# Performance work log

Measured on AMD Instinct MI355X. Metric: run time of the kernel, lower is better.

## Reference

```python
import jax, jax.numpy as jnp
import numpy as np

B, N, E = 4, 10000, 160000
F_EXOG = 8
IN_DIM = 9          # 1 (pm25) + F_EXOG
HIST, PRED = 8, 12
HID = 64
GNN_OUT = 13
E_HID, E_OUT = 32, 30
GRU_IN = IN_DIM + GNN_OUT  # 22


def setup_inputs() -> dict:
    key = jax.random.key(0)
    ks = jax.random.split(key, 16)
    s = 0.1
    return {
        "pm25_hist": jax.random.normal(ks[0], (B, HIST, N, 1), jnp.float32),
        "feature": jax.random.normal(ks[1], (B, HIST + PRED, N, F_EXOG), jnp.float32),
        "edge_attr": jax.random.uniform(ks[2], (E, 2), jnp.float32),
        "wind_mean": jnp.array([2.0, 180.0], jnp.float32),
        "wind_std": jnp.array([1.5, 90.0], jnp.float32),
        # edge MLP: Linear(21->32), Sigmoid, Linear(32->30), Sigmoid
        "e_w1": jax.random.normal(ks[3], (2 * IN_DIM + 3, E_HID), jnp.float32) * s,
        "e_b1": jnp.zeros((E_HID,), jnp.float32),
        "e_w2": jax.random.normal(ks[4], (E_HID, E_OUT), jnp.float32) * s,
        "e_b2": jnp.zeros((E_OUT,), jnp.float32),
        # node MLP: Linear(30->13), Sigmoid
        "n_w": jax.random.normal(ks[5], (E_OUT, GNN_OUT), jnp.float32) * s,
        "n_b": jnp.zeros((GNN_OUT,), jnp.float32),
        # GRUCell(22 -> 64), torch layout: weight_ih (3H, in), weight_hh (3H, H)
        "gru_wi": jax.random.normal(ks[6], (3 * HID, GRU_IN), jnp.float32) * s,
        "gru_wh": jax.random.normal(ks[7], (3 * HID, HID), jnp.float32) * s,
        "gru_bi": jnp.zeros((3 * HID,), jnp.float32),
        "gru_bh": jnp.zeros((3 * HID,), jnp.float32),
        # fc_out: Linear(64 -> 1)
        "fc_w": jax.random.normal(ks[8], (HID, 1), jnp.float32) * s,
        "fc_b": jnp.zeros((1,), jnp.float32),
        "edge_index": jax.random.randint(ks[9], (2, E), 0, N, jnp.int64),
    }


def _forward(pm25_hist, feature, edge_attr, wind_mean, wind_std,
             e_w1, e_b1, e_w2, e_b2, n_w, n_b,
             gru_wi, gru_wh, gru_bi, gru_bh, fc_w, fc_b, edge_index):
    batch, _, n_nodes, _ = pm25_hist.shape
    src, tgt = edge_index[0], edge_index[1]

    # buffers precomputed in __init__ (torch.std uses ddof=1)
    edge_mean = edge_attr.mean(axis=0, keepdims=True)
    edge_std = jnp.maximum(jnp.std(edge_attr, axis=0, ddof=1, keepdims=True), 1e-6)
    edge_attr_norm = (edge_attr - edge_mean) / edge_std          # (E, 2)
    city_dist = jnp.maximum(edge_attr[:, 0], 1e-3)               # (E,)
    city_direc = edge_attr[:, 1]                                 # (E,)
    w_std = jnp.maximum(wind_std, 1e-6)

    def graph_gnn(x):                                            # x: (B, N, IN_DIM)
        node_src = x[:, src]                                     # (B, E, IN_DIM)
        node_tgt = x[:, tgt]
        wind = node_src[..., -2:] * w_std + wind_mean            # de-normalize
        speed = jnp.maximum(wind[..., 0], 0.0)                   # (B, E)
        wdir = jnp.deg2rad(wind[..., 1])
        theta = jnp.abs(city_direc - wdir)
        edge_w = jax.nn.relu(3.0 * speed * jnp.cos(theta) / city_dist)  # (B, E)
        ean = jnp.broadcast_to(edge_attr_norm, (x.shape[0], E, 2))
        h = jnp.concatenate([node_src, node_tgt, ean, edge_w[..., None]], axis=-1)
        h = jax.nn.sigmoid(h @ e_w1 + e_b1)
        h = jax.nn.sigmoid(h @ e_w2 + e_b2)                      # (B, E, E_OUT)
        agg = jnp.zeros((x.shape[0], n_nodes, E_OUT), x.dtype)
        agg = agg.at[:, tgt].add(h).at[:, src].add(-h)           # scatter add / sub
        return jax.nn.sigmoid(agg @ n_w + n_b)                   # (B, N, GNN_OUT)

    def gru_step(h, x):                                          # h,x: (B*N, .)
        gi = x @ gru_wi.T + gru_bi
        gh = h @ gru_wh.T + gru_bh
        i_r, i_z, i_n = jnp.split(gi, 3, axis=-1)
        h_r, h_z, h_n = jnp.split(gh, 3, axis=-1)
        r = jax.nn.sigmoid(i_r + h_r)
        z = jax.nn.sigmoid(i_z + h_z)
        n = jnp.tanh(i_n + r * h_n)
        return (1.0 - z) * n + z * h

    def step(carry, feat_t):
        hn, xn = carry                                           # (B*N,HID), (B,N,1)
        x = jnp.concatenate([xn, feat_t], axis=-1)               # (B, N, IN_DIM)
        x_gnn = graph_gnn(x)
        xc = jnp.concatenate([x_gnn, x], axis=-1).reshape(batch * n_nodes, -1)
        hn = gru_step(hn, xc)
        xn = hn.reshape(batch, n_nodes, HID) @ fc_w + fc_b       # (B, N, 1)
        return (hn, xn), xn[..., 0]

    hn0 = jnp.zeros((batch * n_nodes, HID), pm25_hist.dtype)
    xn0 = pm25_hist[:, -1]                                       # (B, N, 1)
    feats = jnp.swapaxes(feature[:, HIST:HIST + PRED], 0, 1)     # (PRED, B, N, F)
    _, preds = jax.lax.scan(step, (hn0, xn0), feats)             # (PRED, B, N)
    return jnp.transpose(preds, (1, 2, 0))                       # (B, N, PRED)


def reference(pm25_hist, feature, edge_attr, wind_mean, wind_std,
              e_w1, e_b1, e_w2, e_b2, n_w, n_b,
              gru_wi, gru_wh, gru_bi, gru_bh, fc_w, fc_b, edge_index):
    return _forward(pm25_hist, feature, edge_attr, wind_mean, wind_std,
                    e_w1, e_b1, e_w2, e_b2, n_w, n_b,
                    gru_wi, gru_wh, gru_bi, gru_bh, fc_w, fc_b, edge_index)
```

## Files before the change

kernel.cpp:

```cpp
#include <hip/hip_runtime.h>
#include <hip/hip_fp16.h>
#include <cstddef>

#define BB    4
#define NN    10000
#define EE    160000
#define BN    40000
#define HISTC 8
#define PREDC 12
#define TSTEP 20
#define FEX   8
#define HIDC  64
#define EHID  32
#define EOUTC 30
#define GOUTC 13
#define GINC  22

typedef float v2f __attribute__((ext_vector_type(2)));
typedef _Float16 v2h __attribute__((ext_vector_type(2)));

struct alignas(16) WPack {
    __half2 w[16];
    float   nw[14];
    float   b2;
    float   pad;
};

__device__ __forceinline__ float fast_rcp(float x) { return __builtin_amdgcn_rcpf(x); }
__device__ __forceinline__ float sigm(float x) {
    return fast_rcp(1.0f + __expf(-x));
}
__device__ __forceinline__ v2f sigm2(v2f x) {
    v2f r; r.x = sigm(x.x); r.y = sigm(x.y); return r;
}
__device__ __forceinline__ float tanh_fast(float x) {
    x = fminf(fmaxf(x, -15.0f), 15.0f);
    float e = __expf(2.0f * x);
    return (e - 1.0f) * fast_rcp(e + 1.0f);
}

__device__ __forceinline__ float dot2(__half2 a, __half2 b, float c) {
#if __has_builtin(__builtin_amdgcn_fdot2)
    union { __half2 h; v2h v; } ua, ub;
    ua.h = a; ub.h = b;
    return __builtin_amdgcn_fdot2(ua.v, ub.v, c, false);
#else
    float2 fa = __half22float2(a), fb = __half22float2(b);
    return c + fa.x * fb.x + fa.y * fb.y;
#endif
}

__global__ __launch_bounds__(256) void stats1_kernel(const float* __restrict__ ea,
                                                     double* __restrict__ part) {
    __shared__ double sm[256][4];
    int tid = threadIdx.x;
    double s0 = 0, s1 = 0, q0 = 0, q1 = 0;
    for (int e = blockIdx.x * 256 + tid; e < EE; e += 256 * 256) {
        float2 v = reinterpret_cast<const float2*>(ea)[e];
        double v0 = (double)v.x, v1 = (double)v.y;
        s0 += v0; q0 += v0 * v0;
        s1 += v1; q1 += v1 * v1;
    }
    sm[tid][0] = s0; sm[tid][1] = s1; sm[tid][2] = q0; sm[tid][3] = q1;
    __syncthreads();
    for (int off = 128; off > 0; off >>= 1) {
        if (tid < off)
            for (int k = 0; k < 4; k++) sm[tid][k] += sm[tid + off][k];
        __syncthreads();
    }
    if (tid == 0) {
        part[blockIdx.x * 4 + 0] = sm[0][0];
        part[blockIdx.x * 4 + 1] = sm[0][1];
        part[blockIdx.x * 4 + 2] = sm[0][2];
        part[blockIdx.x * 4 + 3] = sm[0][3];
    }
}

__global__ __launch_bounds__(256) void stats2_kernel(const double* __restrict__ part,
                                                     float* __restrict__ stats) {
    __shared__ double sm[256][4];
    int tid = threadIdx.x;
    sm[tid][0] = part[tid * 4 + 0];
    sm[tid][1] = part[tid * 4 + 1];
    sm[tid][2] = part[tid * 4 + 2];
    sm[tid][3] = part[tid * 4 + 3];
    __syncthreads();
    for (int off = 128; off > 0; off >>= 1) {
        if (tid < off)
            for (int k = 0; k < 4; k++) sm[tid][k] += sm[tid + off][k];
        __syncthreads();
    }
    if (tid == 0) {
        double m0 = sm[0][0] / EE, m1 = sm[0][1] / EE;
        double v0 = (sm[0][2] - sm[0][0] * sm[0][0] / EE) / (double)(EE - 1);
        double v1 = (sm[0][3] - sm[0][1] * sm[0][1] / EE) / (double)(EE - 1);
        float sd0 = fmaxf((float)sqrt(v0 > 0 ? v0 : 0.0), 1e-6f);
        float sd1 = fmaxf((float)sqrt(v1 > 0 ? v1 : 0.0), 1e-6f);
        stats[0] = (float)m0; stats[1] = (float)m1;
        stats[2] = 1.0f / sd0; stats[3] = 1.0f / sd1;
    }
}

__global__ __launch_bounds__(256) void edgepre_kernel(
    const float* __restrict__ ea, const float* __restrict__ stats,
    const int* __restrict__ eidx,
    int* __restrict__ deg_t, int* __restrict__ deg_s,
    float4* __restrict__ epre4)
{
    int e = blockIdx.x * 256 + threadIdx.x;
    if (e >= EE) return;
    float2 v = reinterpret_cast<const float2*>(ea)[e];
    float4 r;
    r.x = (v.x - stats[0]) * stats[2];
    r.y = (v.y - stats[1]) * stats[3];
    r.z = 1.0f / fmaxf(v.x, 1e-3f);
    r.w = v.y;
    epre4[e] = r;
    atomicAdd(&deg_s[eidx[e]], 1);
    atomicAdd(&deg_t[eidx[EE + e]], 1);
}

__global__ __launch_bounds__(256) void cvtw_kernel(
    const float* __restrict__ wi, const float* __restrict__ wh,
    const float* __restrict__ ew2, const float* __restrict__ eb2,
    const float* __restrict__ nw,
    __half* __restrict__ wi_h, __half* __restrict__ wh_h,
    WPack* __restrict__ wpack)
{
    int i = blockIdx.x * 256 + threadIdx.x;
    if (i < 192 * GINC) wi_h[i] = __float2half(wi[i]);
    if (i < 192 * HIDC) wh_h[i] = __float2half(wh[i]);
    if (i < EOUTC) {
        WPack wp;
        #pragma unroll
        for (int q = 0; q < 16; q++)
            wp.w[q] = __floats2half2_rn(ew2[(2 * q) * EOUTC + i],
                                        ew2[(2 * q + 1) * EOUTC + i]);
        #pragma unroll
        for (int j = 0; j < GOUTC; j++) wp.nw[j] = nw[i * GOUTC + j];
        wp.nw[13] = 0.f;
        wp.b2 = eb2[i];
        wp.pad = 0.f;
        wpack[i] = wp;
    }
}

__global__ void initxn_kernel(const float* __restrict__ pm, float* __restrict__ xn) {
    int i = blockIdx.x * 256 + threadIdx.x;
    if (i >= BN) return;
    int b = i / NN, n = i - b * NN;
    xn[i] = pm[(b * HISTC + (HISTC - 1)) * NN + n];
}

__global__ __launch_bounds__(1024) void scan_kernel(
    const int* __restrict__ deg_t, const int* __restrict__ deg_s,
    int* __restrict__ off_t, int* __restrict__ off_s,
    int* __restrict__ cnt_t, int* __restrict__ cnt_s)
{
    __shared__ int pt[1024], ps[1024];
    int tid = threadIdx.x;
    int base = tid * 10;
    int st = 0, ss = 0;
    for (int k = 0; k < 10; k++) {
        int i = base + k;
        if (i < NN) { st += deg_t[i]; ss += deg_s[i]; }
    }
    pt[tid] = st; ps[tid] = ss;
    __syncthreads();
    for (int off = 1; off < 1024; off <<= 1) {
        int vt = (tid >= off) ? pt[tid - off] : 0;
        int vs = (tid >= off) ? ps[tid - off] : 0;
        __syncthreads();
        pt[tid] += vt; ps[tid] += vs;
        __syncthreads();
    }
    int ext = (tid == 0) ? 0 : pt[tid - 1];
    int exs = (tid == 0) ? 0 : ps[tid - 1];
    for (int k = 0; k < 10; k++) {
        int i = base + k;
        if (i < NN) {
            off_t[i] = ext; cnt_t[i] = ext;
            off_s[i] = exs; cnt_s[i] = exs;
            ext += deg_t[i]; exs += deg_s[i];
        }
    }
    if (tid == 0) { off_t[NN] = EE; off_s[NN] = EE; }
}

__global__ void fillperm_kernel(const int* __restrict__ eidx,
                                const float4* __restrict__ epre4,
                                int* __restrict__ cnt_t, int* __restrict__ cnt_s,
                                int4* __restrict__ eT, float4* __restrict__ epreT)
{
    int e = blockIdx.x * 256 + threadIdx.x;
    if (e >= EE) return;
    int s = eidx[e];
    int g = eidx[EE + e];
    int pt = atomicAdd(&cnt_t[g], 1);
    int ps = atomicAdd(&cnt_s[s], 1);
    int4 r; r.x = s; r.y = g; r.z = ps; r.w = 0;
    eT[pt] = r;
    epreT[pt] = epre4[e];
}

__global__ __launch_bounds__(256) void featpre_kernel(
    const float* __restrict__ feature,
    const float* __restrict__ ew1,
    const float* __restrict__ wmean, const float* __restrict__ wstd,
    __half* __restrict__ preSfeat, __half* __restrict__ preTfeat,
    float2* __restrict__ wind2all)
{
    __shared__ alignas(16) float w1s[18 * EHID];
    for (int i = threadIdx.x; i < 18 * EHID; i += 256) w1s[i] = ew1[i];
    __syncthreads();
    int idx = blockIdx.x * 256 + threadIdx.x;
    if (idx >= BN * 8 * PREDC) return;
    int c  = idx & 7;
    int r2 = idx >> 3;
    int t  = r2 / BN;
    int i  = r2 - t * BN;
    int b = i / NN, n = i - b * NN;
    float xf[8];
    {
        const float4* fp = reinterpret_cast<const float4*>(
            feature + (((size_t)b * TSTEP + HISTC + t) * NN + n) * FEX);
        float4 u = fp[0], v = fp[1];
        xf[0] = u.x; xf[1] = u.y; xf[2] = u.z; xf[3] = u.w;
        xf[4] = v.x; xf[5] = v.y; xf[6] = v.z; xf[7] = v.w;
    }
    float4 aS = {0.f, 0.f, 0.f, 0.f}, aT = {0.f, 0.f, 0.f, 0.f};
    #pragma unroll
    for (int k = 0; k < 8; k++) {
        float4 wS = reinterpret_cast<const float4*>(&w1s[(k + 1) * EHID])[c];
        float4 wT = reinterpret_cast<const float4*>(&w1s[(10 + k) * EHID])[c];
        aS.x += xf[k] * wS.x; aS.y += xf[k] * wS.y; aS.z += xf[k] * wS.z; aS.w += xf[k] * wS.w;
        aT.x += xf[k] * wT.x; aT.y += xf[k] * wT.y; aT.z += xf[k] * wT.z; aT.w += xf[k] * wT.w;
    }
    union { uint2 u; __half h[4]; } sv, tv;
    sv.h[0] = __float2half(aS.x); sv.h[1] = __float2half(aS.y);
    sv.h[2] = __float2half(aS.z); sv.h[3] = __float2half(aS.w);
    tv.h[0] = __float2half(aT.x); tv.h[1] = __float2half(aT.y);
    tv.h[2] = __float2half(aT.z); tv.h[3] = __float2half(aT.w);
    size_t base = ((size_t)t * BN + i) * EHID;
    reinterpret_cast<uint2*>(preSfeat + base)[c] = sv.u;
    reinterpret_cast<uint2*>(preTfeat + base)[c] = tv.u;
    if (c == 1) {
        float sd0 = fmaxf(wstd[0], 1e-6f), sd1 = fmaxf(wstd[1], 1e-6f);
        float speed = fmaxf(xf[6] * sd0 + wmean[0], 0.f);
        float wdir  = (xf[7] * sd1 + wmean[1]) * 0.017453292519943295f;
        float2 wv; wv.x = 3.0f * speed; wv.y = wdir;
        wind2all[(size_t)t * BN + i] = wv;
    }
}

__global__ __launch_bounds__(256) void edge_kernel(
    const int4* __restrict__ eT, const float4* __restrict__ epreT,
    const __half* __restrict__ preSfeat, const __half* __restrict__ preTfeat,
    const float2* __restrict__ wind2all, int t,
    const float* __restrict__ xncur,
    const float* __restrict__ ew1, const float* __restrict__ eb1,
    const WPack* __restrict__ wpack,
    __half* __restrict__ h3t, __half* __restrict__ h3s)
{
    int i = blockIdx.x * 256 + threadIdx.x;
    int b = blockIdx.y;
    int4 et = eT[i];
    int s = et.x, g = et.y, ps = et.z;
    float4 ep = epreT[i];

    size_t iS = (size_t)b * NN + s, iT = (size_t)b * NN + g;
    size_t tb = (size_t)t * BN;
    float2 wv2 = wind2all[tb + iS];
    float ew = fmaxf(wv2.x * __cosf(fabsf(ep.w - wv2.y)) * ep.z, 0.f);
    float xnS = xncur[iS], xnT = xncur[iT];

    union alignas(16) { uint4 u[4]; __half2 h2[16]; } RS, RT;
    {
        const uint4* p;
        p = reinterpret_cast<const uint4*>(preSfeat + (tb + iS) * EHID);
        RS.u[0] = p[0]; RS.u[1] = p[1]; RS.u[2] = p[2]; RS.u[3] = p[3];
        p = reinterpret_cast<const uint4*>(preTfeat + (tb + iT) * EHID);
        RT.u[0] = p[0]; RT.u[1] = p[1]; RT.u[2] = p[2]; RT.u[3] = p[3];
    }

    const v2f* W00 = reinterpret_cast<const v2f*>(ew1);
    const v2f* W09 = reinterpret_cast<const v2f*>(ew1 + 9 * EHID);
    const v2f* W18 = reinterpret_cast<const v2f*>(ew1 + 18 * EHID);
    const v2f* W19 = reinterpret_cast<const v2f*>(ew1 + 19 * EHID);
    const v2f* W20 = reinterpret_cast<const v2f*>(ew1 + 20 * EHID);
    const v2f* B1  = reinterpret_cast<const v2f*>(eb1);
    float ean0 = ep.x, ean1 = ep.y;
    __half2 h1h[16];
    #pragma unroll
    for (int q = 0; q < 16; q++) {
        v2f u = W18[q] * ean0 + W19[q] * ean1 + B1[q] + W20[q] * ew
              + W00[q] * xnS + W09[q] * xnT;
        float2 rs = __half22float2(RS.h2[q]);
        float2 rt = __half22float2(RT.h2[q]);
        u.x += rs.x + rt.x;
        u.y += rs.y + rt.y;
        v2f sg = sigm2(u);
        h1h[q] = __floats2half2_rn(sg.x, sg.y);
    }

    v2f h3p[7];
    #pragma unroll
    for (int j = 0; j < 7; j++) { h3p[j].x = 0.f; h3p[j].y = 0.f; }
    for (int o = 0; o < EOUTC; o++) {
        const WPack* W = wpack + o;
        float acc0 = W->b2, acc1 = 0.f;
        #pragma unroll
        for (int q = 0; q < 16; q += 2) {
            acc0 = dot2(h1h[q],     W->w[q],     acc0);
            acc1 = dot2(h1h[q + 1], W->w[q + 1], acc1);
        }
        float h2v = sigm(acc0 + acc1);
        const v2f* nr = reinterpret_cast<const v2f*>(W->nw);
        #pragma unroll
        for (int j = 0; j < 7; j++) h3p[j] += nr[j] * h2v;
    }

    union alignas(16) { uint4 u[2]; __half2 h2[8]; } r;
    #pragma unroll
    for (int j = 0; j < 7; j++) r.h2[j] = __floats2half2_rn(h3p[j].x, h3p[j].y);
    r.h2[7] = __floats2half2_rn(0.f, 0.f);
    {
        __half* oT = h3t + ((size_t)b * EE + i) * 16;
        reinterpret_cast<uint4*>(oT)[0] = r.u[0];
        reinterpret_cast<uint4*>(oT)[1] = r.u[1];
        __half* oS = h3s + ((size_t)b * EE + ps) * 16;
        reinterpret_cast<uint4*>(oS)[0] = r.u[0];
        reinterpret_cast<uint4*>(oS)[1] = r.u[1];
    }
}

__global__ __launch_bounds__(256) void gathernode_kernel(
    const __half* __restrict__ h3t, const __half* __restrict__ h3s,
    const int* __restrict__ off_t, const int* __restrict__ off_s,
    const float* __restrict__ nb,
    const float* __restrict__ feature, int t,
    const __half* __restrict__ wi_h, const __half* __restrict__ wh_h,
    const float* __restrict__ bi, const float* __restrict__ bh,
    const float* __restrict__ fw, const float* __restrict__ fb,
    const __half2* __restrict__ hnold, __half2* __restrict__ hnnew,
    float* __restrict__ xncur, float* __restrict__ out)
{
    __shared__ alignas(16) __half xcs[16][4][16];
    __shared__ float xpart[4][64];
    int tid = threadIdx.x;
    int n0 = blockIdx.x * 16;

    {
        int l = tid & 63;
        int gb = l >> 4, ch = l & 15;
        int wv = tid >> 6;
        const __half* ht = h3t + (size_t)gb * ((size_t)EE * 16) + ch;
        const __half* hs = h3s + (size_t)gb * ((size_t)EE * 16) + ch;
        for (int rr = 0; rr < 4; rr++) {
            int ln = rr * 4 + wv;
            int n = __builtin_amdgcn_readfirstlane(n0 + ln);
            float a0 = 0.f, a1 = 0.f, a2 = 0.f, a3 = 0.f;
            {
                int i0 = off_t[n], i1 = off_t[n + 1];
                int i = i0;
                for (; i + 4 <= i1; i += 4) {
                    a0 += __half2float(ht[(size_t)(i + 0) * 16]);
                    a1 += __half2float(ht[(size_t)(i + 1) * 16]);
                    a2 += __half2float(ht[(size_t)(i + 2) * 16]);
                    a3 += __half2float(ht[(size_t)(i + 3) * 16]);
                }
                for (; i < i1; i++) a0 += __half2float(ht[(size_t)i * 16]);
            }
            {
                int i0 = off_s[n], i1 = off_s[n + 1];
                int i = i0;
                for (; i + 4 <= i1; i += 4) {
                    a0 -= __half2float(hs[(size_t)(i + 0) * 16]);
                    a1 -= __half2float(hs[(size_t)(i + 1) * 16]);
                    a2 -= __half2float(hs[(size_t)(i + 2) * 16]);
                    a3 -= __half2float(hs[(size_t)(i + 3) * 16]);
                }
                for (; i < i1; i++) a0 -= __half2float(hs[(size_t)i * 16]);
            }
            float acc = (a0 + a1) + (a2 + a3);
            __half v = (ch < GOUTC) ? __float2half(sigm(acc + nb[ch]))
                                    : __float2half(0.f);
            xcs[ln][gb][ch] = v;
        }
    }
    __syncthreads();

    int lane = tid & 63, wav = tid >> 6;
    int nn = lane & 15, b = lane >> 4;
    int node = b * NN + n0 + nn;
    float xn_old = xncur[node];

    __half2 xch[11];
    {
        const __half2* xp2 = reinterpret_cast<const __half2*>(&xcs[nn][b][0]);
        #pragma unroll
        for (int p = 0; p < 6; p++) xch[p] = xp2[p];
        xch[6] = __halves2half2(xcs[nn][b][12], __float2half(xn_old));
    }
    {
        const float4* fp = reinterpret_cast<const float4*>(
            feature + (((size_t)b * TSTEP + HISTC + t) * NN + (n0 + nn)) * FEX);
        float4 u = fp[0], v = fp[1];
        xch[7]  = __floats2half2_rn(u.x, u.y);
        xch[8]  = __floats2half2_rn(u.z, u.w);
        xch[9]  = __floats2half2_rn(v.x, v.y);
        xch[10] = __floats2half2_rn(v.z, v.w);
    }

    __half2 hh[32];
    #pragma unroll
    for (int p = 0; p < 32; p++) hh[p] = hnold[(size_t)p * BN + node];

    float xsum = 0.f;
    for (int jb = 0; jb < 4; jb++) {
        #pragma unroll
        for (int jj2 = 0; jj2 < 2; jj2++) {
            int j0 = __builtin_amdgcn_readfirstlane(jb * 16 + wav * 4 + jj2 * 2);
            union { __half2 h; __half v[2]; } holdw;
            holdw.h = hnold[(size_t)(j0 >> 1) * BN + node];
            float hnew2[2];
            #pragma unroll
            for (int d = 0; d < 2; d++) {
                int j = j0 + d;
                float ir = bi[j], iz = bi[64 + j], in_ = bi[128 + j];
                const __half2* wr0 = reinterpret_cast<const __half2*>(wi_h + (size_t)j * GINC);
                const __half2* wr1 = reinterpret_cast<const __half2*>(wi_h + (size_t)(64 + j) * GINC);
                const __half2* wr2 = reinterpret_cast<const __half2*>(wi_h + (size_t)(128 + j) * GINC);
                #pragma unroll
                for (int p = 0; p < 11; p++) {
                    ir  = dot2(xch[p], wr0[p], ir);
                    iz  = dot2(xch[p], wr1[p], iz);
                    in_ = dot2(xch[p], wr2[p], in_);
                }
                float hr0 = bh[j], hz0 = bh[64 + j], hn0 = bh[128 + j];
                float hr1 = 0.f, hz1 = 0.f, hn1 = 0.f;
                const __half2* vr0 = reinterpret_cast<const __half2*>(wh_h + (size_t)j * HIDC);
                const __half2* vr1 = reinterpret_cast<const __half2*>(wh_h + (size_t)(64 + j) * HIDC);
                const __half2* vr2 = reinterpret_cast<const __half2*>(wh_h + (size_t)(128 + j) * HIDC);
                #pragma unroll
                for (int p = 0; p < 32; p += 2) {
                    hr0 = dot2(hh[p],     vr0[p],     hr0);
                    hz0 = dot2(hh[p],     vr1[p],     hz0);
                    hn0 = dot2(hh[p],     vr2[p],     hn0);
                    hr1 = dot2(hh[p + 1], vr0[p + 1], hr1);
                    hz1 = dot2(hh[p + 1], vr1[p + 1], hz1);
                    hn1 = dot2(hh[p + 1], vr2[p + 1], hn1);
                }
                float r  = sigm(ir + hr0 + hr1);
                float z  = sigm(iz + hz0 + hz1);
                float nl = tanh_fast(in_ + r * (hn0 + hn1));
                float hold = __half2float(holdw.v[d]);
                float hnew = (1.f - z) * nl + z * hold;
                hnew2[d] = hnew;
                xsum += hnew * fw[j];
            }
            hnnew[(size_t)(j0 >> 1) * BN + node] = __floats2half2_rn(hnew2[0], hnew2[1]);
        }
    }
    xpart[wav][lane] = xsum;
    __syncthreads();
    if (wav == 0) {
        float tot = xpart[0][lane] + xpart[1][lane] + xpart[2][lane] + xpart[3][lane];
        float xnew = tot + fb[0];
        xncur[node] = xnew;
        out[(size_t)node * PREDC + t] = xnew;
    }
}

extern "C" void kernel_launch(void* const* d_in, const int* in_sizes, int n_in,
                              void* d_out, int out_size, void* d_ws, size_t ws_size,
                              hipStream_t stream)
{
    const float* pm    = (const float*)d_in[0];
    const float* feat  = (const float*)d_in[1];
    const float* ea    = (const float*)d_in[2];
    const float* wmean = (const float*)d_in[3];
    const float* wstd  = (const float*)d_in[4];
    const float* ew1   = (const float*)d_in[5];
    const float* eb1   = (const float*)d_in[6];
    const float* ew2   = (const float*)d_in[7];
    const float* eb2   = (const float*)d_in[8];
    const float* nw    = (const float*)d_in[9];
    const float* nb    = (const float*)d_in[10];
    const float* wi    = (const float*)d_in[11];
    const float* wh    = (const float*)d_in[12];
    const float* bi    = (const float*)d_in[13];
    const float* bh    = (const float*)d_in[14];
    const float* fw    = (const float*)d_in[15];
    const float* fb    = (const float*)d_in[16];
    const int*   eidx  = (const int*)d_in[17];
    float* out = (float*)d_out;

    char* w = (char*)d_ws;
    double* partd = (double*)w;                    w += 256 * 4 * sizeof(double);
    float*  stats = (float*)w;                     w += 16 * sizeof(float);
    WPack*  wpack = (WPack*)w;                     w += EOUTC * sizeof(WPack);
    float4* epre4 = (float4*)w;                    w += (size_t)EE * sizeof(float4);
    float4* epreT = (float4*)w;                    w += (size_t)EE * sizeof(float4);
    float*  xncur = (float*)w;                     w += (size_t)BN * sizeof(float);
    __half2* hnA  = (__half2*)w;                   w += (size_t)32 * BN * sizeof(__half2);
    __half2* hnB  = (__half2*)w;                   w += (size_t)32 * BN * sizeof(__half2);
    __half* preSfeat = (__half*)w;                 w += (size_t)PREDC * BN * EHID * sizeof(__half);
    __half* preTfeat = (__half*)w;                 w += (size_t)PREDC * BN * EHID * sizeof(__half);
    float2* wind2all = (float2*)w;                 w += (size_t)PREDC * BN * sizeof(float2);
    __half* h3t   = (__half*)w;                    w += (size_t)BB * EE * 16 * sizeof(__half);
    __half* h3s   = (__half*)w;                    w += (size_t)BB * EE * 16 * sizeof(__half);
    __half* wi_h  = (__half*)w;                    w += (size_t)192 * GINC * sizeof(__half);
    __half* wh_h  = (__half*)w;                    w += (size_t)192 * HIDC * sizeof(__half);
    int4*   eT    = (int4*)w;                      w += (size_t)EE * sizeof(int4);
    int*    deg_t = (int*)w;                       w += NN * sizeof(int);
    int*    deg_s = (int*)w;                       w += NN * sizeof(int);
    int*    off_t = (int*)w;                       w += (NN + 1) * sizeof(int);
    int*    off_s = (int*)w;                       w += (NN + 1) * sizeof(int);
    int*    cnt_t = (int*)w;                       w += NN * sizeof(int);
    int*    cnt_s = (int*)w;                       w += NN * sizeof(int);

    stats1_kernel<<<256, 256, 0, stream>>>(ea, partd);
    stats2_kernel<<<1, 256, 0, stream>>>(partd, stats);
    hipMemsetAsync(deg_t, 0, 2 * NN * sizeof(int), stream);
    edgepre_kernel<<<(EE + 255) / 256, 256, 0, stream>>>(
        ea, stats, eidx, deg_t, deg_s, epre4);
    cvtw_kernel<<<(192 * HIDC + 255) / 256, 256, 0, stream>>>(
        wi, wh, ew2, eb2, nw, wi_h, wh_h, wpack);
    initxn_kernel<<<(BN + 255) / 256, 256, 0, stream>>>(pm, xncur);
    hipMemsetAsync(hnA, 0, (size_t)32 * BN * sizeof(__half2), stream);
    scan_kernel<<<1, 1024, 0, stream>>>(deg_t, deg_s, off_t, off_s, cnt_t, cnt_s);
    fillperm_kernel<<<(EE + 255) / 256, 256, 0, stream>>>(
        eidx, epre4, cnt_t, cnt_s, eT, epreT);
    featpre_kernel<<<(BN * 8 * PREDC + 255) / 256, 256, 0, stream>>>(
        feat, ew1, wmean, wstd, preSfeat, preTfeat, wind2all);

    for (int t = 0; t < PREDC; t++) {
        const __half2* hnold = (t & 1) ? hnB : hnA;
        __half2*       hnnew = (t & 1) ? hnA : hnB;
        edge_kernel<<<dim3(EE / 256, BB), 256, 0, stream>>>(
            eT, epreT, preSfeat, preTfeat, wind2all, t, xncur,
            ew1, eb1, wpack, h3t, h3s);
        gathernode_kernel<<<NN / 16, 256, 0, stream>>>(
            h3t, h3s, off_t, off_s, nb, feat, t, wi_h, wh_h, bi, bh,
            fw, fb, hnold, hnnew, xncur, out);
    }
}
```

Baseline: 1.145 ms.

## Split gather and GRU node work into separate kernels; stage edge weights in LDS

The fused gather+GRU kernel becomes two kernels. A gather kernel uses one wavefront per node and writes the aggregated GNN features plus the current pm25 value to a small fp16 buffer. A node kernel then runs the GRU with 512 threads per 64 nodes, so each wave handles 8 hidden units, and it reuses the old hidden state already loaded in registers. The edge kernel also copies its MLP weights into shared memory, so the weight reads come from LDS instead of global/scalar loads. This adds an extra launch and a round trip through the intermediate buffer per step, in exchange for better parallelism in the GRU stage.

```diff
diff --git a/kernel.cpp b/kernel.cpp
--- a/kernel.cpp
+++ b/kernel.cpp
@@ -262,6 +262,20 @@
     const WPack* __restrict__ wpack,
     __half* __restrict__ h3t, __half* __restrict__ h3s)
 {
+    __shared__ alignas(16) WPack swp[EOUTC];
+    __shared__ alignas(16) float sw1[6 * EHID];
+    {
+        const uint4* src = reinterpret_cast<const uint4*>(wpack);
+        uint4* dst = reinterpret_cast<uint4*>(swp);
+        for (int k = threadIdx.x; k < EOUTC * 8; k += 256) dst[k] = src[k];
+        if (threadIdx.x < 192) {
+            int r = threadIdx.x >> 5, c = threadIdx.x & 31;
+            int row = (r == 0) ? 0 : ((r == 1) ? 9 : 16 + r);
+            sw1[threadIdx.x] = (r < 5) ? ew1[row * EHID + c] : eb1[c];
+        }
+    }
+    __syncthreads();
+
     int i = blockIdx.x * 256 + threadIdx.x;
     int b = blockIdx.y;
     int4 et = eT[i];
@@ -283,12 +297,12 @@
         RT.u[0] = p[0]; RT.u[1] = p[1]; RT.u[2] = p[2]; RT.u[3] = p[3];
     }
 
-    const v2f* W00 = reinterpret_cast<const v2f*>(ew1);
-    const v2f* W09 = reinterpret_cast<const v2f*>(ew1 + 9 * EHID);
-    const v2f* W18 = reinterpret_cast<const v2f*>(ew1 + 18 * EHID);
-    const v2f* W19 = reinterpret_cast<const v2f*>(ew1 + 19 * EHID);
-    const v2f* W20 = reinterpret_cast<const v2f*>(ew1 + 20 * EHID);
-    const v2f* B1  = reinterpret_cast<const v2f*>(eb1);
+    const v2f* W00 = reinterpret_cast<const v2f*>(sw1);
+    const v2f* W09 = reinterpret_cast<const v2f*>(sw1 + EHID);
+    const v2f* W18 = reinterpret_cast<const v2f*>(sw1 + 2 * EHID);
+    const v2f* W19 = reinterpret_cast<const v2f*>(sw1 + 3 * EHID);
+    const v2f* W20 = reinterpret_cast<const v2f*>(sw1 + 4 * EHID);
+    const v2f* B1  = reinterpret_cast<const v2f*>(sw1 + 5 * EHID);
     float ean0 = ep.x, ean1 = ep.y;
     __half2 h1h[16];
     #pragma unroll
@@ -307,7 +321,7 @@
     #pragma unroll
     for (int j = 0; j < 7; j++) { h3p[j].x = 0.f; h3p[j].y = 0.f; }
     for (int o = 0; o < EOUTC; o++) {
-        const WPack* W = wpack + o;
+        const WPack* W = swp + o;
         float acc0 = W->b2, acc1 = 0.f;
         #pragma unroll
         for (int q = 0; q < 16; q += 2) {
@@ -334,77 +348,81 @@
     }
 }
 
-__global__ __launch_bounds__(256) void gathernode_kernel(
+__global__ __launch_bounds__(256) void gather_kernel(
     const __half* __restrict__ h3t, const __half* __restrict__ h3s,
     const int* __restrict__ off_t, const int* __restrict__ off_s,
-    const float* __restrict__ nb,
-    const float* __restrict__ feature, int t,
+    const float* __restrict__ nb, const float* __restrict__ xncur,
+    __half* __restrict__ xcagg)
+{
+    int n = (blockIdx.x * 256 + threadIdx.x) >> 6;
+    if (n >= NN) return;
+    n = __builtin_amdgcn_readfirstlane(n);
+    int lane = threadIdx.x & 63;
+    int b = lane >> 4, ch = lane & 15;
+    const __half* ht = h3t + (size_t)b * EE * 16 + ch;
+    const __half* hs = h3s + (size_t)b * EE * 16 + ch;
+    float a0 = 0.f, a1 = 0.f, a2 = 0.f, a3 = 0.f;
+    {
+        int i0 = off_t[n], i1 = off_t[n + 1];
+        int i = i0;
+        for (; i + 4 <= i1; i += 4) {
+            a0 += __half2float(ht[(size_t)(i + 0) * 16]);
+            a1 += __half2float(ht[(size_t)(i + 1) * 16]);
+            a2 += __half2float(ht[(size_t)(i + 2) * 16]);
+            a3 += __half2float(ht[(size_t)(i + 3) * 16]);
+        }
+        for (; i < i1; i++) a0 += __half2float(ht[(size_t)i * 16]);
+    }
+    {
+        int i0 = off_s[n], i1 = off_s[n + 1];
+        int i = i0;
+        for (; i + 4 <= i1; i += 4) {
+            a0 -= __half2float(hs[(size_t)(i + 0) * 16]);
+            a1 -= __half2float(hs[(size_t)(i + 1) * 16]);
+            a2 -= __half2float(hs[(size_t)(i + 2) * 16]);
+            a3 -= __half2float(hs[(size_t)(i + 3) * 16]);
+        }
+        for (; i < i1; i++) a0 -= __half2float(hs[(size_t)i * 16]);
+    }
+    float acc = (a0 + a1) + (a2 + a3);
+    float val;
+    if (ch < GOUTC) {
+        val = sigm(acc + nb[ch]);
+    } else if (ch == GOUTC) {
+        val = xncur[(size_t)b * NN + n];
+    } else {
+        val = 0.f;
+    }
+    xcagg[((size_t)b * NN + n) * 16 + ch] = __float2half(val);
+}
+
+__global__ __launch_bounds__(512, 4) void node_kernel(
+    const __half* __restrict__ xcagg, const float* __restrict__ feature, int t,
     const __half* __restrict__ wi_h, const __half* __restrict__ wh_h,
     const float* __restrict__ bi, const float* __restrict__ bh,
     const float* __restrict__ fw, const float* __restrict__ fb,
     const __half2* __restrict__ hnold, __half2* __restrict__ hnnew,
     float* __restrict__ xncur, float* __restrict__ out)
 {
-    __shared__ alignas(16) __half xcs[16][4][16];
-    __shared__ float xpart[4][64];
-    int tid = threadIdx.x;
-    int n0 = blockIdx.x * 16;
-
-    {
-        int l = tid & 63;
-        int gb = l >> 4, ch = l & 15;
-        int wv = tid >> 6;
-        const __half* ht = h3t + (size_t)gb * ((size_t)EE * 16) + ch;
-        const __half* hs = h3s + (size_t)gb * ((size_t)EE * 16) + ch;
-        for (int rr = 0; rr < 4; rr++) {
-            int ln = rr * 4 + wv;
-            int n = __builtin_amdgcn_readfirstlane(n0 + ln);
-            float a0 = 0.f, a1 = 0.f, a2 = 0.f, a3 = 0.f;
-            {
-                int i0 = off_t[n], i1 = off_t[n + 1];
-                int i = i0;
-                for (; i + 4 <= i1; i += 4) {
-                    a0 += __half2float(ht[(size_t)(i + 0) * 16]);
-                    a1 += __half2float(ht[(size_t)(i + 1) * 16]);
-                    a2 += __half2float(ht[(size_t)(i + 2) * 16]);
-                    a3 += __half2float(ht[(size_t)(i + 3) * 16]);
-                }
-                for (; i < i1; i++) a0 += __half2float(ht[(size_t)i * 16]);
-            }
-            {
-                int i0 = off_s[n], i1 = off_s[n + 1];
-                int i = i0;
-                for (; i + 4 <= i1; i += 4) {
-                    a0 -= __half2float(hs[(size_t)(i + 0) * 16]);
-                    a1 -= __half2float(hs[(size_t)(i + 1) * 16]);
-                    a2 -= __half2float(hs[(size_t)(i + 2) * 16]);
-                    a3 -= __half2float(hs[(size_t)(i + 3) * 16]);
-                }
-                for (; i < i1; i++) a0 -= __half2float(hs[(size_t)i * 16]);
-            }
-            float acc = (a0 + a1) + (a2 + a3);
-            __half v = (ch < GOUTC) ? __float2half(sigm(acc + nb[ch]))
-                                    : __float2half(0.f);
-            xcs[ln][gb][ch] = v;
-        }
-    }
-    __syncthreads();
-
-    int lane = tid & 63, wav = tid >> 6;
-    int nn = lane & 15, b = lane >> 4;
-    int node = b * NN + n0 + nn;
-    float xn_old = xncur[node];
+    __shared__ float xpart[8][64];
+    int tid  = threadIdx.x;
+    int lane = tid & 63;
+    int wav  = tid >> 6;
+    int node = blockIdx.x * 64 + lane;
+    int b = node / NN;
+    int n = node - b * NN;
 
     __half2 xch[11];
     {
-        const __half2* xp2 = reinterpret_cast<const __half2*>(&xcs[nn][b][0]);
-        #pragma unroll
-        for (int p = 0; p < 6; p++) xch[p] = xp2[p];
-        xch[6] = __halves2half2(xcs[nn][b][12], __float2half(xn_old));
+        union alignas(16) { uint4 u[2]; __half2 h2[8]; } X;
+        const uint4* xp16 = reinterpret_cast<const uint4*>(xcagg + (size_t)node * 16);
+        X.u[0] = xp16[0]; X.u[1] = xp16[1];
+        #pragma unroll
+        for (int p = 0; p < 7; p++) xch[p] = X.h2[p];
     }
     {
         const float4* fp = reinterpret_cast<const float4*>(
-            feature + (((size_t)b * TSTEP + HISTC + t) * NN + (n0 + nn)) * FEX);
+            feature + (((size_t)b * TSTEP + HISTC + t) * NN + n) * FEX);
         float4 u = fp[0], v = fp[1];
         xch[7]  = __floats2half2_rn(u.x, u.y);
         xch[8]  = __floats2half2_rn(u.z, u.w);
@@ -416,59 +434,59 @@
     #pragma unroll
     for (int p = 0; p < 32; p++) hh[p] = hnold[(size_t)p * BN + node];
 
+    float hnew8[8];
     float xsum = 0.f;
-    for (int jb = 0; jb < 4; jb++) {
-        #pragma unroll
-        for (int jj2 = 0; jj2 < 2; jj2++) {
-            int j0 = __builtin_amdgcn_readfirstlane(jb * 16 + wav * 4 + jj2 * 2);
-            union { __half2 h; __half v[2]; } holdw;
-            holdw.h = hnold[(size_t)(j0 >> 1) * BN + node];
-            float hnew2[2];
-            #pragma unroll
-            for (int d = 0; d < 2; d++) {
-                int j = j0 + d;
-                float ir = bi[j], iz = bi[64 + j], in_ = bi[128 + j];
-                const __half2* wr0 = reinterpret_cast<const __half2*>(wi_h + (size_t)j * GINC);
-                const __half2* wr1 = reinterpret_cast<const __half2*>(wi_h + (size_t)(64 + j) * GINC);
-                const __half2* wr2 = reinterpret_cast<const __half2*>(wi_h + (size_t)(128 + j) * GINC);
-                #pragma unroll
-                for (int p = 0; p < 11; p++) {
-                    ir  = dot2(xch[p], wr0[p], ir);
-                    iz  = dot2(xch[p], wr1[p], iz);
-                    in_ = dot2(xch[p], wr2[p], in_);
-                }
-                float hr0 = bh[j], hz0 = bh[64 + j], hn0 = bh[128 + j];
-                float hr1 = 0.f, hz1 = 0.f, hn1 = 0.f;
-                const __half2* vr0 = reinterpret_cast<const __half2*>(wh_h + (size_t)j * HIDC);
-                const __half2* vr1 = reinterpret_cast<const __half2*>(wh_h + (size_t)(64 + j) * HIDC);
-                const __half2* vr2 = reinterpret_cast<const __half2*>(wh_h + (size_t)(128 + j) * HIDC);
-                #pragma unroll
-                for (int p = 0; p < 32; p += 2) {
-                    hr0 = dot2(hh[p],     vr0[p],     hr0);
-                    hz0 = dot2(hh[p],     vr1[p],     hz0);
-                    hn0 = dot2(hh[p],     vr2[p],     hn0);
-                    hr1 = dot2(hh[p + 1], vr0[p + 1], hr1);
-                    hz1 = dot2(hh[p + 1], vr1[p + 1], hz1);
-                    hn1 = dot2(hh[p + 1], vr2[p + 1], hn1);
-                }
-                float r  = sigm(ir + hr0 + hr1);
-                float z  = sigm(iz + hz0 + hz1);
-                float nl = tanh_fast(in_ + r * (hn0 + hn1));
-                float hold = __half2float(holdw.v[d]);
-                float hnew = (1.f - z) * nl + z * hold;
-                hnew2[d] = hnew;
-                xsum += hnew * fw[j];
-            }
-            hnnew[(size_t)(j0 >> 1) * BN + node] = __floats2half2_rn(hnew2[0], hnew2[1]);
-        }
+    #pragma unroll
+    for (int d = 0; d < 8; d++) {
+        int j = __builtin_amdgcn_readfirstlane(wav * 8 + d);
+        float ir = bi[j], iz = bi[64 + j], in_ = bi[128 + j];
+        const __half2* wr0 = reinterpret_cast<const __half2*>(wi_h + (size_t)j * GINC);
+        const __half2* wr1 = reinterpret_cast<const __half2*>(wi_h + (size_t)(64 + j) * GINC);
+        const __half2* wr2 = reinterpret_cast<const __half2*>(wi_h + (size_t)(128 + j) * GINC);
+        #pragma unroll
+        for (int p = 0; p < 11; p++) {
+            ir  = dot2(xch[p], wr0[p], ir);
+            iz  = dot2(xch[p], wr1[p], iz);
+            in_ = dot2(xch[p], wr2[p], in_);
+        }
+        float hr0 = bh[j], hz0 = bh[64 + j], hn0 = bh[128 + j];
+        float hr1 = 0.f, hz1 = 0.f, hn1 = 0.f;
+        const __half2* vr0 = reinterpret_cast<const __half2*>(wh_h + (size_t)j * HIDC);
+        const __half2* vr1 = reinterpret_cast<const __half2*>(wh_h + (size_t)(64 + j) * HIDC);
+        const __half2* vr2 = reinterpret_cast<const __half2*>(wh_h + (size_t)(128 + j) * HIDC);
+        #pragma unroll
+        for (int p = 0; p < 32; p += 2) {
+            hr0 = dot2(hh[p],     vr0[p],     hr0);
+            hz0 = dot2(hh[p],     vr1[p],     hz0);
+            hn0 = dot2(hh[p],     vr2[p],     hn0);
+            hr1 = dot2(hh[p + 1], vr0[p + 1], hr1);
+            hz1 = dot2(hh[p + 1], vr1[p + 1], hz1);
+            hn1 = dot2(hh[p + 1], vr2[p + 1], hn1);
+        }
+        float r  = sigm(ir + hr0 + hr1);
+        float z  = sigm(iz + hz0 + hz1);
+        float nl = tanh_fast(in_ + r * (hn0 + hn1));
+        union { __half2 h; __half v[2]; } hold2;
+        hold2.h = hh[(wav * 8 + d) >> 1];
+        float hold = __half2float(hold2.v[d & 1]);
+        float hnew = (1.f - z) * nl + z * hold;
+        hnew8[d] = hnew;
+        xsum += hnew * fw[j];
+    }
+    #pragma unroll
+    for (int q = 0; q < 4; q++) {
+        hnnew[(size_t)(wav * 4 + q) * BN + node] =
+            __floats2half2_rn(hnew8[2 * q], hnew8[2 * q + 1]);
     }
     xpart[wav][lane] = xsum;
     __syncthreads();
-    if (wav == 0) {
-        float tot = xpart[0][lane] + xpart[1][lane] + xpart[2][lane] + xpart[3][lane];
+    if (tid < 64) {
+        float tot = ((xpart[0][tid] + xpart[1][tid]) + (xpart[2][tid] + xpart[3][tid]))
+                  + ((xpart[4][tid] + xpart[5][tid]) + (xpart[6][tid] + xpart[7][tid]));
+        int node2 = blockIdx.x * 64 + tid;
         float xnew = tot + fb[0];
-        xncur[node] = xnew;
-        out[(size_t)node * PREDC + t] = xnew;
+        xncur[node2] = xnew;
+        out[(size_t)node2 * PREDC + t] = xnew;
     }
 }
 
@@ -505,6 +523,7 @@
     float*  xncur = (float*)w;                     w += (size_t)BN * sizeof(float);
     __half2* hnA  = (__half2*)w;                   w += (size_t)32 * BN * sizeof(__half2);
     __half2* hnB  = (__half2*)w;                   w += (size_t)32 * BN * sizeof(__half2);
+    __half* xcagg = (__half*)w;                    w += (size_t)BN * 16 * sizeof(__half);
     __half* preSfeat = (__half*)w;                 w += (size_t)PREDC * BN * EHID * sizeof(__half);
     __half* preTfeat = (__half*)w;                 w += (size_t)PREDC * BN * EHID * sizeof(__half);
     float2* wind2all = (float2*)w;                 w += (size_t)PREDC * BN * sizeof(float2);
@@ -541,8 +560,10 @@
         edge_kernel<<<dim3(EE / 256, BB), 256, 0, stream>>>(
             eT, epreT, preSfeat, preTfeat, wind2all, t, xncur,
             ew1, eb1, wpack, h3t, h3s);
-        gathernode_kernel<<<NN / 16, 256, 0, stream>>>(
-            h3t, h3s, off_t, off_s, nb, feat, t, wi_h, wh_h, bi, bh,
-            fw, fb, hnold, hnnew, xncur, out);
-    }
-}
+        gather_kernel<<<(NN * 64 + 255) / 256, 256, 0, stream>>>(
+            h3t, h3s, off_t, off_s, nb, xncur, xcagg);
+        node_kernel<<<BN / 64, 512, 0, stream>>>(
+            xcagg, feat, t, wi_h, wh_h, bi, bh, fw, fb,
+            hnold, hnnew, xncur, out);
+    }
+}
```

Result: slower. 1.261 ms (+10.1%).
